# Performance work log

Measured on AMD Instinct MI355X. Metric: run time of the kernel, lower is better.

## Reference

```python
import jax, jax.numpy as jnp
import numpy as np

NUM_HEADS = 16
EPS = 1e-6
NEG_INF = -1e9


def layer_norm(x, scale, bias):
    m = jnp.mean(x, axis=-1, keepdims=True)
    v = jnp.mean(jnp.square(x - m), axis=-1, keepdims=True)
    return (x - m) * jax.lax.rsqrt(v + EPS) * scale + bias


def mha(x_q, x_kv, wq, wk, wv, wo, causal):
    B, Sq, D = x_q.shape
    Sk = x_kv.shape[1]
    H = NUM_HEADS
    Dh = D // H
    q = (x_q @ wq).reshape(B, Sq, H, Dh) * (1.0 / np.sqrt(Dh))
    k = (x_kv @ wk).reshape(B, Sk, H, Dh)
    v = (x_kv @ wv).reshape(B, Sk, H, Dh)
    scores = jnp.einsum('bqhf,bkhf->bhqk', q, k)  # [B,H,Sq,Sk]
    if causal:
        mask = jnp.tril(jnp.ones((Sq, Sk), dtype=bool))
        scores = jnp.where(mask, scores, NEG_INF)
    p = jax.nn.softmax(scores, axis=-1)
    o = jnp.einsum('bhqk,bkhf->bqhf', p, v).reshape(B, Sq, D)
    return o @ wo


def setup_inputs() -> dict:
    key = jax.random.key(0)
    ks = jax.random.split(key, 12)
    B, S, D, F = 2, 2048, 1024, 4096
    w = 0.02
    return {
        'targets': jax.random.normal(ks[0], (B, S, D), jnp.float32),
        'encoded': jax.random.normal(ks[1], (B, S, D), jnp.float32),
        'ln1_s': jnp.ones((D,), jnp.float32),
        'ln1_b': jnp.zeros((D,), jnp.float32),
        'sa_wq': jax.random.normal(ks[2], (D, D), jnp.float32) * w,
        'sa_wk': jax.random.normal(ks[3], (D, D), jnp.float32) * w,
        'sa_wv': jax.random.normal(ks[4], (D, D), jnp.float32) * w,
        'sa_wo': jax.random.normal(ks[5], (D, D), jnp.float32) * w,
        'ln2_s': jnp.ones((D,), jnp.float32),
        'ln2_b': jnp.zeros((D,), jnp.float32),
        'ca_wq': jax.random.normal(ks[6], (D, D), jnp.float32) * w,
        'ca_wk': jax.random.normal(ks[7], (D, D), jnp.float32) * w,
        'ca_wv': jax.random.normal(ks[8], (D, D), jnp.float32) * w,
        'ca_wo': jax.random.normal(ks[9], (D, D), jnp.float32) * w,
        'ln3_s': jnp.ones((D,), jnp.float32),
        'ln3_b': jnp.zeros((D,), jnp.float32),
        'mlp_w1': jax.random.normal(ks[10], (D, F), jnp.float32) * w,
        'mlp_b1': jnp.zeros((F,), jnp.float32),
        'mlp_w2': jax.random.normal(ks[11], (F, D), jnp.float32) * w,
        'mlp_b2': jnp.zeros((D,), jnp.float32),
    }


def reference(targets, encoded, ln1_s, ln1_b, sa_wq, sa_wk, sa_wv, sa_wo,
              ln2_s, ln2_b, ca_wq, ca_wk, ca_wv, ca_wo,
              ln3_s, ln3_b, mlp_w1, mlp_b1, mlp_w2, mlp_b2):
    # Pre-LN causal self-attention + residual
    x = layer_norm(targets, ln1_s, ln1_b)
    x = mha(x, x, sa_wq, sa_wk, sa_wv, sa_wo, causal=True)
    x = x + targets
    # Pre-LN cross-attention over encoder output + residual
    y = layer_norm(x, ln2_s, ln2_b)
    y = mha(y, encoded, ca_wq, ca_wk, ca_wv, ca_wo, causal=False)
    y = y + x
    # Pre-LN MLP + residual
    z = layer_norm(y, ln3_s, ln3_b)
    z = jax.nn.relu(z @ mlp_w1 + mlp_b1) @ mlp_w2 + mlp_b2
    return y + z
```

## Files before the change

### kernel.cpp

```cpp
#include <hip/hip_runtime.h>


#define DEV __device__ __forceinline__

typedef __attribute__((ext_vector_type(8))) _Float16 half8;
typedef __attribute__((ext_vector_type(4))) _Float16 half4;
typedef __attribute__((ext_vector_type(4))) float    f32x4;

#define GLB(p) ((const __attribute__((address_space(1))) void*)(p))
#define LDS(p) ((__attribute__((address_space(3))) void*)(p))

DEV float wave_sum_f(float v) {
  #pragma unroll
  for (int off = 32; off; off >>= 1) v += __shfl_xor(v, off);
  return v;
}

struct WtArgs { const float* w[8]; _Float16* wt[8]; };

__global__ __launch_bounds__(256) void wt_square(WtArgs a) {
  const float* w = a.w[blockIdx.z];
  _Float16* wt = a.wt[blockIdx.z];
  __shared__ float t[32][33];
  const int tx = threadIdx.x, ty = threadIdx.y;
  const int n0 = blockIdx.x * 32, k0 = blockIdx.y * 32;
  #pragma unroll
  for (int i = ty; i < 32; i += 8)
    t[i][tx] = w[(size_t)(k0 + i) * 1024 + n0 + tx];
  __syncthreads();
  #pragma unroll
  for (int i = ty; i < 32; i += 8)
    wt[(size_t)(n0 + i) * 1024 + k0 + tx] = (_Float16)t[tx][i];
}

__global__ __launch_bounds__(256) void wt_one(const float* __restrict__ w,
                                              _Float16* __restrict__ wt,
                                              int K, int N) {
  __shared__ float t[32][33];
  const int tx = threadIdx.x, ty = threadIdx.y;
  const int n0 = blockIdx.x * 32, k0 = blockIdx.y * 32;
  #pragma unroll
  for (int i = ty; i < 32; i += 8)
    t[i][tx] = w[(size_t)(k0 + i) * N + n0 + tx];
  __syncthreads();
  #pragma unroll
  for (int i = ty; i < 32; i += 8)
    wt[(size_t)(n0 + i) * K + k0 + tx] = (_Float16)t[tx][i];
}

__global__ __launch_bounds__(256) void cvt_f16(const float* __restrict__ in,
                                               _Float16* __restrict__ out) {
  const size_t i = ((size_t)blockIdx.x * 256 + threadIdx.x) * 4;
  const float4 v = *(const float4*)(in + i);
  half4 o;
  o.x = (_Float16)v.x; o.y = (_Float16)v.y; o.z = (_Float16)v.z; o.w = (_Float16)v.w;
  *(half4*)(out + i) = o;
}

__global__ __launch_bounds__(256) void ln_kernel(const float* __restrict__ x,
                                                 const float* __restrict__ sc,
                                                 const float* __restrict__ bi,
                                                 _Float16* __restrict__ out) {
  const int row = blockIdx.x;
  const int t = threadIdx.x;
  const float4 v = ((const float4*)(x + (size_t)row * 1024))[t];
  float s  = v.x + v.y + v.z + v.w;
  float s2 = v.x * v.x + v.y * v.y + v.z * v.z + v.w * v.w;
  s = wave_sum_f(s); s2 = wave_sum_f(s2);
  __shared__ float red[8];
  const int lane = t & 63, wid = t >> 6;
  if (lane == 0) { red[wid] = s; red[4 + wid] = s2; }
  __syncthreads();
  s  = red[0] + red[1] + red[2] + red[3];
  s2 = red[4] + red[5] + red[6] + red[7];
  const float mean = s * (1.f / 1024.f);
  const float rstd = rsqrtf(s2 * (1.f / 1024.f) - mean * mean + 1e-6f);
  const float4 sv = ((const float4*)sc)[t];
  const float4 bv = ((const float4*)bi)[t];
  half4 o;
  o.x = (_Float16)((v.x - mean) * rstd * sv.x + bv.x);
  o.y = (_Float16)((v.y - mean) * rstd * sv.y + bv.y);
  o.z = (_Float16)((v.z - mean) * rstd * sv.z + bv.z);
  o.w = (_Float16)((v.w - mean) * rstd * sv.w + bv.w);
  ((half4*)(out + (size_t)row * 1024))[t] = o;
}

template <int EPI, int BM, int BN>
__global__ __launch_bounds__(256)
void gemm_f16(const _Float16* __restrict__ A, const _Float16* __restrict__ Bt,
              void* __restrict__ Cout, const float* __restrict__ bias,
              const float* __restrict__ resid, int M, int N, int K,
              float scl, int sclCols) {
  constexpr int BK = 64;
  constexpr int AM = BM / 32;
  constexpr int AN = BN / 32;
  __shared__ _Float16 As[BM * BK];
  __shared__ _Float16 Bs[BN * BK];
  const int tid = threadIdx.x;
  const int lane = tid & 63, wid = tid >> 6;
  const int wm = wid >> 1, wn = wid & 1;
  const int q = lane >> 4, m15 = lane & 15;
  const int bm = blockIdx.y, bn = blockIdx.x;

  const _Float16* Ab = A + (size_t)bm * BM * K + (size_t)(tid >> 3) * K + (tid & 7) * 8;
  const _Float16* Bb = Bt + (size_t)bn * BN * K + (size_t)(tid >> 3) * K + (tid & 7) * 8;

  f32x4 acc[AM][AN] = {};

  for (int k0 = 0; k0 < K; k0 += BK) {
    if (k0) __syncthreads();
    #pragma unroll
    for (int r = 0; r < BM / 32; r++)
      __builtin_amdgcn_global_load_lds(GLB(Ab + (size_t)r * 32 * K + k0),
                                       LDS(&As[r * 2048 + wid * 512]), 16, 0, 0);
    #pragma unroll
    for (int r = 0; r < BN / 32; r++)
      __builtin_amdgcn_global_load_lds(GLB(Bb + (size_t)r * 32 * K + k0),
                                       LDS(&Bs[r * 2048 + wid * 512]), 16, 0, 0);
    __syncthreads();
    #pragma unroll
    for (int kk = 0; kk < 2; kk++) {
      half8 af[AM], bf[AN];
      #pragma unroll
      for (int i = 0; i < AM; i++)
        af[i] = *(const half8*)&As[(wm * (BM / 2) + i * 16 + m15) * BK + kk * 32 + q * 8];
      #pragma unroll
      for (int i = 0; i < AN; i++)
        bf[i] = *(const half8*)&Bs[(wn * (BN / 2) + i * 16 + m15) * BK + kk * 32 + q * 8];
      #pragma unroll
      for (int mi = 0; mi < AM; mi++)
        #pragma unroll
        for (int ni = 0; ni < AN; ni++)
          acc[mi][ni] = __builtin_amdgcn_mfma_f32_16x16x32_f16(af[mi], bf[ni],
                                                               acc[mi][ni], 0, 0, 0);
    }
  }

  const int rowbase = bm * BM + wm * (BM / 2);
  const int colbase = bn * BN + wn * (BN / 2);
  #pragma unroll
  for (int ni = 0; ni < AN; ni++) {
    const int col = colbase + ni * 16 + m15;
    float bv = 0.f;
    if (EPI == 2 || EPI == 4) bv = bias[col];
    const float cs = (EPI == 1) ? (col < sclCols ? scl : 1.f) : 1.f;
    #pragma unroll
    for (int mi = 0; mi < AM; mi++) {
      #pragma unroll
      for (int r = 0; r < 4; r++) {
        const int row = rowbase + mi * 16 + q * 4 + r;
        const size_t idx = (size_t)row * N + col;
        float v = acc[mi][ni][r];
        if (EPI == 1) {
          ((_Float16*)Cout)[idx] = (_Float16)(v * cs);
        } else if (EPI == 2) {
          v += bv; v = v > 0.f ? v : 0.f;
          ((_Float16*)Cout)[idx] = (_Float16)v;
        } else if (EPI == 3) {
          ((float*)Cout)[idx] = v + resid[idx];
        } else {
          ((float*)Cout)[idx] = v + bv + resid[idx];
        }
      }
    }
  }
}

__global__ __launch_bounds__(256) void kt_kernel(const _Float16* __restrict__ src,
                                                 int srcStride,
                                                 _Float16* __restrict__ Kt, int S) {
  const int bh = blockIdx.z;
  const int b = bh >> 4, h = bh & 15;
  const int s0 = blockIdx.x * 32, d0 = blockIdx.y * 32;
  __shared__ _Float16 t[32][33];
  const int tx = threadIdx.x, ty = threadIdx.y;
  #pragma unroll
  for (int i = ty; i < 32; i += 8)
    t[i][tx] = src[(size_t)(b * S + s0 + i) * srcStride + h * 64 + d0 + tx];
  __syncthreads();
  #pragma unroll
  for (int i = ty; i < 32; i += 8)
    Kt[((size_t)bh * 64 + d0 + i) * S + s0 + tx] = t[tx][i];
}

__global__ __launch_bounds__(256)
void flash_attn(const _Float16* __restrict__ Q, int qs,
                const _Float16* __restrict__ Kp, int ks,
                const _Float16* __restrict__ Vt, _Float16* __restrict__ O,
                int S, int Sk, int causal) {
  __shared__ _Float16 Ks[64 * 72];
  __shared__ _Float16 Vs[64 * 72];
  __shared__ _Float16 Pq[4][32 * 72];
  const int tid = threadIdx.x;
  const int lane = tid & 63, wid = tid >> 6;
  const int quad = lane >> 4, c15 = lane & 15;
  const int h = blockIdx.y, b = blockIdx.z;
  int qb = blockIdx.x;
  if (causal) qb = (qb & 1) ? ((int)gridDim.x - 1 - (qb >> 1)) : (qb >> 1);
  const int qw0 = qb * 128 + wid * 32;

  half8 qf[2][2];
  #pragma unroll
  for (int nt = 0; nt < 2; nt++)
    #pragma unroll
    for (int kk = 0; kk < 2; kk++)
      qf[nt][kk] = *(const half8*)(Q + (size_t)(b * S + qw0 + nt * 16 + c15) * qs +
                                   h * 64 + kk * 32 + quad * 8);

  f32x4 oacc[4][2];
  #pragma unroll
  for (int i = 0; i < 4; i++)
    #pragma unroll
    for (int j = 0; j < 2; j++)
      oacc[i][j] = (f32x4){0.f, 0.f, 0.f, 0.f};
  float lpart[2] = {0.f, 0.f};

  const int ntiles = causal ? (qb * 2 + 2) : (Sk >> 6);
  const _Float16* Kg = Kp + (size_t)b * Sk * ks + h * 64;
  const _Float16* Vg = Vt + (size_t)(b * 16 + h) * 64 * Sk;

  const int srow = tid >> 3, sg8 = (tid & 7) * 8;
  half8 rk0, rk1, rv0, rv1;
  auto ldkv = [&](int jb) {
    rk0 = *(const half8*)(Kg + (size_t)(jb + srow) * ks + sg8);
    rk1 = *(const half8*)(Kg + (size_t)(jb + srow + 32) * ks + sg8);
    rv0 = *(const half8*)(Vg + (size_t)srow * Sk + jb + sg8);
    rv1 = *(const half8*)(Vg + (size_t)(srow + 32) * Sk + jb + sg8);
  };
  ldkv(0);

  for (int t = 0; t < ntiles; t++) {
    const int jb = t * 64;
    __syncthreads();
    *(half8*)&Ks[srow * 72 + sg8] = rk0;
    *(half8*)&Ks[(srow + 32) * 72 + sg8] = rk1;
    *(half8*)&Vs[srow * 72 + sg8] = rv0;
    *(half8*)&Vs[(srow + 32) * 72 + sg8] = rv1;
    __syncthreads();
    if (t + 1 < ntiles) ldkv(jb + 64);
    if (causal && jb > qw0 + 31) continue;

    f32x4 s[4][2];
    #pragma unroll
    for (int mt = 0; mt < 4; mt++) {
      const half8 kf0 = *(const half8*)&Ks[(mt * 16 + c15) * 72 + quad * 8];
      const half8 kf1 = *(const half8*)&Ks[(mt * 16 + c15) * 72 + 32 + quad * 8];
      #pragma unroll
      for (int nt = 0; nt < 2; nt++) {
        f32x4 z = {0.f, 0.f, 0.f, 0.f};
        z = __builtin_amdgcn_mfma_f32_16x16x32_f16(kf0, qf[nt][0], z, 0, 0, 0);
        z = __builtin_amdgcn_mfma_f32_16x16x32_f16(kf1, qf[nt][1], z, 0, 0, 0);
        s[mt][nt] = z;
      }
    }

    if (causal && jb + 63 > qw0) {
      #pragma unroll
      for (int mt = 0; mt < 4; mt++)
        #pragma unroll
        for (int nt = 0; nt < 2; nt++) {
          const int qglob = qw0 + nt * 16 + c15;
          #pragma unroll
          for (int rr = 0; rr < 4; rr++) {
            const int kglob = jb + mt * 16 + quad * 4 + rr;
            if (kglob > qglob) s[mt][nt][rr] = -1e30f;
          }
        }
    }

    #pragma unroll
    for (int nt = 0; nt < 2; nt++) {
      float psum = 0.f;
      #pragma unroll
      for (int mt = 0; mt < 4; mt++) {
        #pragma unroll
        for (int rr = 0; rr < 4; rr++) {
          const float p = exp2f(s[mt][nt][rr]);
          s[mt][nt][rr] = p;
          psum += p;
        }
      }
      lpart[nt] += psum;
      #pragma unroll
      for (int mtk = 0; mtk < 4; mtk++) {
        half4 ph;
        ph.x = (_Float16)s[mtk][nt][0]; ph.y = (_Float16)s[mtk][nt][1];
        ph.z = (_Float16)s[mtk][nt][2]; ph.w = (_Float16)s[mtk][nt][3];
        *(half4*)&Pq[wid][(nt * 16 + c15) * 72 + mtk * 16 + quad * 4] = ph;
      }
    }

    half8 pb[2][2];
    #pragma unroll
    for (int kk = 0; kk < 2; kk++)
      #pragma unroll
      for (int nt = 0; nt < 2; nt++)
        pb[kk][nt] = *(const half8*)&Pq[wid][(nt * 16 + c15) * 72 + kk * 32 + quad * 8];
    #pragma unroll
    for (int mtd = 0; mtd < 4; mtd++) {
      const half8 vf0 = *(const half8*)&Vs[(mtd * 16 + c15) * 72 + quad * 8];
      const half8 vf1 = *(const half8*)&Vs[(mtd * 16 + c15) * 72 + 32 + quad * 8];
      #pragma unroll
      for (int nt = 0; nt < 2; nt++) {
        oacc[mtd][nt] = __builtin_amdgcn_mfma_f32_16x16x32_f16(vf0, pb[0][nt],
                                                               oacc[mtd][nt], 0, 0, 0);
        oacc[mtd][nt] = __builtin_amdgcn_mfma_f32_16x16x32_f16(vf1, pb[1][nt],
                                                               oacc[mtd][nt], 0, 0, 0);
      }
    }
  }

  #pragma unroll
  for (int nt = 0; nt < 2; nt++) {
    float l = lpart[nt];
    l += __shfl_xor(l, 16);
    l += __shfl_xor(l, 32);
    const float linv = 1.f / l;
    #pragma unroll
    for (int mtd = 0; mtd < 4; mtd++) {
      half4 ov;
      ov.x = (_Float16)(oacc[mtd][nt][0] * linv);
      ov.y = (_Float16)(oacc[mtd][nt][1] * linv);
      ov.z = (_Float16)(oacc[mtd][nt][2] * linv);
      ov.w = (_Float16)(oacc[mtd][nt][3] * linv);
      *(half4*)(O + (size_t)(b * S + qw0 + nt * 16 + c15) * 1024 +
                h * 64 + mtd * 16 + quad * 4) = ov;
    }
  }
}

extern "C" void kernel_launch(void* const* d_in, const int* in_sizes, int n_in,
                              void* d_out, int out_size, void* d_ws, size_t ws_size,
                              hipStream_t stream) {
  const float* targets = (const float*)d_in[0];
  const float* encoded = (const float*)d_in[1];
  const float* ln1_s = (const float*)d_in[2];
  const float* ln1_b = (const float*)d_in[3];
  const float* sa_wq = (const float*)d_in[4];
  const float* sa_wk = (const float*)d_in[5];
  const float* sa_wv = (const float*)d_in[6];
  const float* sa_wo = (const float*)d_in[7];
  const float* ln2_s = (const float*)d_in[8];
  const float* ln2_b = (const float*)d_in[9];
  const float* ca_wq = (const float*)d_in[10];
  const float* ca_wk = (const float*)d_in[11];
  const float* ca_wv = (const float*)d_in[12];
  const float* ca_wo = (const float*)d_in[13];
  const float* ln3_s = (const float*)d_in[14];
  const float* ln3_b = (const float*)d_in[15];
  const float* mlp_w1 = (const float*)d_in[16];
  const float* mlp_b1 = (const float*)d_in[17];
  const float* mlp_w2 = (const float*)d_in[18];
  const float* mlp_b2 = (const float*)d_in[19];

  const int B = 2, S = 2048, D = 1024, F = 4096, M = B * S;
  const size_t MB = 1024ull * 1024ull;
  const float QSCALE = 0.125f * 1.44269504f;
  char* ws = (char*)d_ws;
  _Float16* wsq   = (_Float16*)(ws);
  _Float16* w1t   = (_Float16*)(ws + 16 * MB);
  _Float16* w2t   = (_Float16*)(ws + 24 * MB);
  _Float16* Abf   = (_Float16*)(ws + 32 * MB);
  _Float16* encbf = (_Float16*)(ws + 40 * MB);
  _Float16* QKV   = (_Float16*)(ws + 48 * MB);
  _Float16* Qcb   = (_Float16*)(ws + 48 * MB);
  _Float16* KVb   = (_Float16*)(ws + 56 * MB);
  _Float16* h1    = (_Float16*)(ws + 48 * MB);
  _Float16* Vtb   = (_Float16*)(ws + 80 * MB);
  _Float16* Aob   = (_Float16*)(ws + 88 * MB);
  float*    xres  = (float*)(ws + 96 * MB);
  float*    yres  = (float*)(ws + 112 * MB);

  {
    WtArgs wa;
    const float* sw[8] = {sa_wq, sa_wk, sa_wv, sa_wo, ca_wq, ca_wk, ca_wv, ca_wo};
    for (int i = 0; i < 8; i++) { wa.w[i] = sw[i]; wa.wt[i] = wsq + (size_t)i * D * D; }
    wt_square<<<dim3(32, 32, 8), dim3(32, 8), 0, stream>>>(wa);
  }
  wt_one<<<dim3(F / 32, D / 32), dim3(32, 8), 0, stream>>>(mlp_w1, w1t, D, F);
  wt_one<<<dim3(D / 32, F / 32), dim3(32, 8), 0, stream>>>(mlp_w2, w2t, F, D);
  cvt_f16<<<(M * D) / 1024, 256, 0, stream>>>(encoded, encbf);

  const dim3 gKT(S / 32, 2, B * 16);
  const dim3 gA(S / 128, 16, B);

  ln_kernel<<<M, 256, 0, stream>>>(targets, ln1_s, ln1_b, Abf);
  gemm_f16<1, 128, 128><<<dim3(3072 / 128, M / 128), 256, 0, stream>>>(
      Abf, wsq, QKV, nullptr, nullptr, M, 3072, D, QSCALE, 1024);
  kt_kernel<<<gKT, dim3(32, 8), 0, stream>>>(QKV + 2048, 3072, Vtb, S);
  flash_attn<<<gA, 256, 0, stream>>>(QKV, 3072, QKV + 1024, 3072, Vtb, Aob, S, S, 1);
  gemm_f16<3, 128, 64><<<dim3(1024 / 64, M / 128), 256, 0, stream>>>(
      Aob, wsq + 3ull * D * D, xres, nullptr, targets, M, D, D, 1.f, 0);

  ln_kernel<<<M, 256, 0, stream>>>(xres, ln2_s, ln2_b, Abf);
  gemm_f16<1, 128, 64><<<dim3(1024 / 64, M / 128), 256, 0, stream>>>(
      Abf, wsq + 4ull * D * D, Qcb, nullptr, nullptr, M, D, D, QSCALE, 1024);
  gemm_f16<1, 128, 128><<<dim3(2048 / 128, M / 128), 256, 0, stream>>>(
      encbf, wsq + 5ull * D * D, KVb, nullptr, nullptr, M, 2048, D, 1.f, 0);
  kt_kernel<<<gKT, dim3(32, 8), 0, stream>>>(KVb + 1024, 2048, Vtb, S);
  flash_attn<<<gA, 256, 0, stream>>>(Qcb, 1024, KVb, 2048, Vtb, Aob, S, S, 0);
  gemm_f16<3, 128, 64><<<dim3(1024 / 64, M / 128), 256, 0, stream>>>(
      Aob, wsq + 7ull * D * D, yres, nullptr, xres, M, D, D, 1.f, 0);

  ln_kernel<<<M, 256, 0, stream>>>(yres, ln3_s, ln3_b, Abf);
  gemm_f16<2, 128, 128><<<dim3(F / 128, M / 128), 256, 0, stream>>>(
      Abf, w1t, h1, mlp_b1, nullptr, M, F, D, 1.f, 0);
  gemm_f16<4, 128, 64><<<dim3(1024 / 64, M / 128), 256, 0, stream>>>(
      h1, w2t, (float*)d_out, mlp_b2, yres, M, D, F, 1.f, 0);

  (void)in_sizes; (void)n_in; (void)out_size; (void)ws_size;
}
```

Baseline: 600.4 us.

## Fuse V transpose into QKV GEMM epilogue and shrink attention blocks to 64 rows

The QKV and cross-attention KV GEMMs gain an epilogue mode that writes the V columns straight into the transposed per-head layout, so the separate kt_kernel launches and their global round trip go away. Flash attention now uses 128-thread blocks covering 64 query rows, which doubles the grid and makes causal tile counts exact instead of idle waves skipping tiles. fp16 conversions use packed round-toward-zero cvt_pkrtz. The transposed V writes from the epilogue are scattered 8-byte stores, and round-toward-zero changes rounding slightly.

```diff
diff --git a/kernel.cpp b/kernel.cpp
--- a/kernel.cpp
+++ b/kernel.cpp
@@ -5,10 +5,20 @@
 
 typedef __attribute__((ext_vector_type(8))) _Float16 half8;
 typedef __attribute__((ext_vector_type(4))) _Float16 half4;
+typedef __attribute__((ext_vector_type(2))) _Float16 half2v;
 typedef __attribute__((ext_vector_type(4))) float    f32x4;
 
 #define GLB(p) ((const __attribute__((address_space(1))) void*)(p))
 #define LDS(p) ((__attribute__((address_space(3))) void*)(p))
+
+DEV half2v pk(float a, float b) {
+  return __builtin_bit_cast(half2v, __builtin_amdgcn_cvt_pkrtz(a, b));
+}
+DEV half4 pk4(float a, float b, float c, float d) {
+  half2v lo = pk(a, b), hi = pk(c, d);
+  half4 r; r.x = lo.x; r.y = lo.y; r.z = hi.x; r.w = hi.y;
+  return r;
+}
 
 DEV float wave_sum_f(float v) {
   #pragma unroll
@@ -52,9 +62,7 @@
                                                _Float16* __restrict__ out) {
   const size_t i = ((size_t)blockIdx.x * 256 + threadIdx.x) * 4;
   const float4 v = *(const float4*)(in + i);
-  half4 o;
-  o.x = (_Float16)v.x; o.y = (_Float16)v.y; o.z = (_Float16)v.z; o.w = (_Float16)v.w;
-  *(half4*)(out + i) = o;
+  *(half4*)(out + i) = pk4(v.x, v.y, v.z, v.w);
 }
 
 __global__ __launch_bounds__(256) void ln_kernel(const float* __restrict__ x,
@@ -77,11 +85,10 @@
   const float rstd = rsqrtf(s2 * (1.f / 1024.f) - mean * mean + 1e-6f);
   const float4 sv = ((const float4*)sc)[t];
   const float4 bv = ((const float4*)bi)[t];
-  half4 o;
-  o.x = (_Float16)((v.x - mean) * rstd * sv.x + bv.x);
-  o.y = (_Float16)((v.y - mean) * rstd * sv.y + bv.y);
-  o.z = (_Float16)((v.z - mean) * rstd * sv.z + bv.z);
-  o.w = (_Float16)((v.w - mean) * rstd * sv.w + bv.w);
+  half4 o = pk4((v.x - mean) * rstd * sv.x + bv.x,
+                (v.y - mean) * rstd * sv.y + bv.y,
+                (v.z - mean) * rstd * sv.z + bv.z,
+                (v.w - mean) * rstd * sv.w + bv.w);
   ((half4*)(out + (size_t)row * 1024))[t] = o;
 }
 
@@ -90,7 +97,7 @@
 void gemm_f16(const _Float16* __restrict__ A, const _Float16* __restrict__ Bt,
               void* __restrict__ Cout, const float* __restrict__ bias,
               const float* __restrict__ resid, int M, int N, int K,
-              float scl, int sclCols) {
+              float scl, int sclCols, _Float16* __restrict__ vt, int vcol0) {
   constexpr int BK = 64;
   constexpr int AM = BM / 32;
   constexpr int AN = BN / 32;
@@ -143,7 +150,19 @@
     const int col = colbase + ni * 16 + m15;
     float bv = 0.f;
     if (EPI == 2 || EPI == 4) bv = bias[col];
-    const float cs = (EPI == 1) ? (col < sclCols ? scl : 1.f) : 1.f;
+    const float cs = (EPI == 1 || EPI == 5) ? (col < sclCols ? scl : 1.f) : 1.f;
+    if (EPI == 5 && col >= vcol0) {
+      const int d = col & 63, hh = (col >> 6) & 15;
+      #pragma unroll
+      for (int mi = 0; mi < AM; mi++) {
+        const int row = rowbase + mi * 16 + q * 4;
+        const int bb = row >> 11, ss = row & 2047;
+        half4 ov = pk4(acc[mi][ni][0], acc[mi][ni][1],
+                       acc[mi][ni][2], acc[mi][ni][3]);
+        *(half4*)(vt + ((size_t)(bb * 16 + hh) * 64 + d) * 2048 + ss) = ov;
+      }
+      continue;
+    }
     #pragma unroll
     for (int mi = 0; mi < AM; mi++) {
       #pragma unroll
@@ -151,7 +170,7 @@
         const int row = rowbase + mi * 16 + q * 4 + r;
         const size_t idx = (size_t)row * N + col;
         float v = acc[mi][ni][r];
-        if (EPI == 1) {
+        if (EPI == 1 || EPI == 5) {
           ((_Float16*)Cout)[idx] = (_Float16)(v * cs);
         } else if (EPI == 2) {
           v += bv; v = v > 0.f ? v : 0.f;
@@ -166,38 +185,21 @@
   }
 }
 
-__global__ __launch_bounds__(256) void kt_kernel(const _Float16* __restrict__ src,
-                                                 int srcStride,
-                                                 _Float16* __restrict__ Kt, int S) {
-  const int bh = blockIdx.z;
-  const int b = bh >> 4, h = bh & 15;
-  const int s0 = blockIdx.x * 32, d0 = blockIdx.y * 32;
-  __shared__ _Float16 t[32][33];
-  const int tx = threadIdx.x, ty = threadIdx.y;
-  #pragma unroll
-  for (int i = ty; i < 32; i += 8)
-    t[i][tx] = src[(size_t)(b * S + s0 + i) * srcStride + h * 64 + d0 + tx];
-  __syncthreads();
-  #pragma unroll
-  for (int i = ty; i < 32; i += 8)
-    Kt[((size_t)bh * 64 + d0 + i) * S + s0 + tx] = t[tx][i];
-}
-
-__global__ __launch_bounds__(256)
+__global__ __launch_bounds__(128)
 void flash_attn(const _Float16* __restrict__ Q, int qs,
                 const _Float16* __restrict__ Kp, int ks,
                 const _Float16* __restrict__ Vt, _Float16* __restrict__ O,
                 int S, int Sk, int causal) {
   __shared__ _Float16 Ks[64 * 72];
   __shared__ _Float16 Vs[64 * 72];
-  __shared__ _Float16 Pq[4][32 * 72];
+  __shared__ _Float16 Pq[2][32 * 72];
   const int tid = threadIdx.x;
   const int lane = tid & 63, wid = tid >> 6;
   const int quad = lane >> 4, c15 = lane & 15;
   const int h = blockIdx.y, b = blockIdx.z;
   int qb = blockIdx.x;
   if (causal) qb = (qb & 1) ? ((int)gridDim.x - 1 - (qb >> 1)) : (qb >> 1);
-  const int qw0 = qb * 128 + wid * 32;
+  const int qw0 = qb * 64 + wid * 32;
 
   half8 qf[2][2];
   #pragma unroll
@@ -215,30 +217,31 @@
       oacc[i][j] = (f32x4){0.f, 0.f, 0.f, 0.f};
   float lpart[2] = {0.f, 0.f};
 
-  const int ntiles = causal ? (qb * 2 + 2) : (Sk >> 6);
+  const int ntiles = causal ? (qb + 1) : (Sk >> 6);
   const _Float16* Kg = Kp + (size_t)b * Sk * ks + h * 64;
   const _Float16* Vg = Vt + (size_t)(b * 16 + h) * 64 * Sk;
 
   const int srow = tid >> 3, sg8 = (tid & 7) * 8;
-  half8 rk0, rk1, rv0, rv1;
+  half8 rk[4], rv[4];
   auto ldkv = [&](int jb) {
-    rk0 = *(const half8*)(Kg + (size_t)(jb + srow) * ks + sg8);
-    rk1 = *(const half8*)(Kg + (size_t)(jb + srow + 32) * ks + sg8);
-    rv0 = *(const half8*)(Vg + (size_t)srow * Sk + jb + sg8);
-    rv1 = *(const half8*)(Vg + (size_t)(srow + 32) * Sk + jb + sg8);
+    #pragma unroll
+    for (int i = 0; i < 4; i++) {
+      rk[i] = *(const half8*)(Kg + (size_t)(jb + srow + i * 16) * ks + sg8);
+      rv[i] = *(const half8*)(Vg + (size_t)(srow + i * 16) * Sk + jb + sg8);
+    }
   };
   ldkv(0);
 
   for (int t = 0; t < ntiles; t++) {
     const int jb = t * 64;
     __syncthreads();
-    *(half8*)&Ks[srow * 72 + sg8] = rk0;
-    *(half8*)&Ks[(srow + 32) * 72 + sg8] = rk1;
-    *(half8*)&Vs[srow * 72 + sg8] = rv0;
-    *(half8*)&Vs[(srow + 32) * 72 + sg8] = rv1;
+    #pragma unroll
+    for (int i = 0; i < 4; i++) {
+      *(half8*)&Ks[(srow + i * 16) * 72 + sg8] = rk[i];
+      *(half8*)&Vs[(srow + i * 16) * 72 + sg8] = rv[i];
+    }
     __syncthreads();
     if (t + 1 < ntiles) ldkv(jb + 64);
-    if (causal && jb > qw0 + 31) continue;
 
     f32x4 s[4][2];
     #pragma unroll
@@ -283,10 +286,8 @@
       lpart[nt] += psum;
       #pragma unroll
       for (int mtk = 0; mtk < 4; mtk++) {
-        half4 ph;
-        ph.x = (_Float16)s[mtk][nt][0]; ph.y = (_Float16)s[mtk][nt][1];
-        ph.z = (_Float16)s[mtk][nt][2]; ph.w = (_Float16)s[mtk][nt][3];
-        *(half4*)&Pq[wid][(nt * 16 + c15) * 72 + mtk * 16 + quad * 4] = ph;
+        *(half4*)&Pq[wid][(nt * 16 + c15) * 72 + mtk * 16 + quad * 4] =
+            pk4(s[mtk][nt][0], s[mtk][nt][1], s[mtk][nt][2], s[mtk][nt][3]);
       }
     }
 
@@ -318,11 +319,8 @@
     const float linv = 1.f / l;
     #pragma unroll
     for (int mtd = 0; mtd < 4; mtd++) {
-      half4 ov;
-      ov.x = (_Float16)(oacc[mtd][nt][0] * linv);
-      ov.y = (_Float16)(oacc[mtd][nt][1] * linv);
-      ov.z = (_Float16)(oacc[mtd][nt][2] * linv);
-      ov.w = (_Float16)(oacc[mtd][nt][3] * linv);
+      half4 ov = pk4(oacc[mtd][nt][0] * linv, oacc[mtd][nt][1] * linv,
+                     oacc[mtd][nt][2] * linv, oacc[mtd][nt][3] * linv);
       *(half4*)(O + (size_t)(b * S + qw0 + nt * 16 + c15) * 1024 +
                 h * 64 + mtd * 16 + quad * 4) = ov;
     }
@@ -381,32 +379,29 @@
   wt_one<<<dim3(D / 32, F / 32), dim3(32, 8), 0, stream>>>(mlp_w2, w2t, F, D);
   cvt_f16<<<(M * D) / 1024, 256, 0, stream>>>(encoded, encbf);
 
-  const dim3 gKT(S / 32, 2, B * 16);
-  const dim3 gA(S / 128, 16, B);
+  const dim3 gA(S / 64, 16, B);
 
   ln_kernel<<<M, 256, 0, stream>>>(targets, ln1_s, ln1_b, Abf);
-  gemm_f16<1, 128, 128><<<dim3(3072 / 128, M / 128), 256, 0, stream>>>(
-      Abf, wsq, QKV, nullptr, nullptr, M, 3072, D, QSCALE, 1024);
-  kt_kernel<<<gKT, dim3(32, 8), 0, stream>>>(QKV + 2048, 3072, Vtb, S);
-  flash_attn<<<gA, 256, 0, stream>>>(QKV, 3072, QKV + 1024, 3072, Vtb, Aob, S, S, 1);
+  gemm_f16<5, 128, 128><<<dim3(3072 / 128, M / 128), 256, 0, stream>>>(
+      Abf, wsq, QKV, nullptr, nullptr, M, 3072, D, QSCALE, 1024, Vtb, 2048);
+  flash_attn<<<gA, 128, 0, stream>>>(QKV, 3072, QKV + 1024, 3072, Vtb, Aob, S, S, 1);
   gemm_f16<3, 128, 64><<<dim3(1024 / 64, M / 128), 256, 0, stream>>>(
-      Aob, wsq + 3ull * D * D, xres, nullptr, targets, M, D, D, 1.f, 0);
+      Aob, wsq + 3ull * D * D, xres, nullptr, targets, M, D, D, 1.f, 0, nullptr, 0);
 
   ln_kernel<<<M, 256, 0, stream>>>(xres, ln2_s, ln2_b, Abf);
   gemm_f16<1, 128, 64><<<dim3(1024 / 64, M / 128), 256, 0, stream>>>(
-      Abf, wsq + 4ull * D * D, Qcb, nullptr, nullptr, M, D, D, QSCALE, 1024);
-  gemm_f16<1, 128, 128><<<dim3(2048 / 128, M / 128), 256, 0, stream>>>(
-      encbf, wsq + 5ull * D * D, KVb, nullptr, nullptr, M, 2048, D, 1.f, 0);
-  kt_kernel<<<gKT, dim3(32, 8), 0, stream>>>(KVb + 1024, 2048, Vtb, S);
-  flash_attn<<<gA, 256, 0, stream>>>(Qcb, 1024, KVb, 2048, Vtb, Aob, S, S, 0);
+      Abf, wsq + 4ull * D * D, Qcb, nullptr, nullptr, M, D, D, QSCALE, 1024, nullptr, 0);
+  gemm_f16<5, 128, 128><<<dim3(2048 / 128, M / 128), 256, 0, stream>>>(
+      encbf, wsq + 5ull * D * D, KVb, nullptr, nullptr, M, 2048, D, 1.f, 0, Vtb, 1024);
+  flash_attn<<<gA, 128, 0, stream>>>(Qcb, 1024, KVb, 2048, Vtb, Aob, S, S, 0);
   gemm_f16<3, 128, 64><<<dim3(1024 / 64, M / 128), 256, 0, stream>>>(
-      Aob, wsq + 7ull * D * D, yres, nullptr, xres, M, D, D, 1.f, 0);
+      Aob, wsq + 7ull * D * D, yres, nullptr, xres, M, D, D, 1.f, 0, nullptr, 0);
 
   ln_kernel<<<M, 256, 0, stream>>>(yres, ln3_s, ln3_b, Abf);
   gemm_f16<2, 128, 128><<<dim3(F / 128, M / 128), 256, 0, stream>>>(
-      Abf, w1t, h1, mlp_b1, nullptr, M, F, D, 1.f, 0);
+      Abf, w1t, h1, mlp_b1, nullptr, M, F, D, 1.f, 0, nullptr, 0);
   gemm_f16<4, 128, 64><<<dim3(1024 / 64, M / 128), 256, 0, stream>>>(
-      h1, w2t, (float*)d_out, mlp_b2, yres, M, D, F, 1.f, 0);
+      h1, w2t, (float*)d_out, mlp_b2, yres, M, D, F, 1.f, 0, nullptr, 0);
 
   (void)in_sizes; (void)n_in; (void)out_size; (void)ws_size;
 }
```

After: 594.0 us. About the same (-1.1%).
